# Kernel optimization log

Measured on AMD Instinct MI355X. Metric: run time of the kernel, lower is better.

## Reference

```python
import jax, jax.numpy as jnp
import numpy as np

N_USERS = 100000
N_ITEMS = 50000
N = N_USERS + N_ITEMS
EMBED_DIM = 64
N_LAYERS = 3
N_EDGES = 4800000


def setup_inputs() -> dict:
    key = jax.random.key(0)
    k1, k2, k3, k4, k5 = jax.random.split(key, 5)
    adj_row = jax.random.randint(k1, (N_EDGES,), 0, N, dtype=jnp.int64 if jax.config.jax_enable_x64 else jnp.int32)
    adj_col = jax.random.randint(k2, (N_EDGES,), 0, N, dtype=jnp.int64 if jax.config.jax_enable_x64 else jnp.int32)
    adj_val = jax.random.uniform(k3, (N_EDGES,), dtype=jnp.float32)
    # learned parameters: nn.init.normal_(std=0.1)
    user_emb = 0.1 * jax.random.normal(k4, (N_USERS, EMBED_DIM), dtype=jnp.float32)
    item_emb = 0.1 * jax.random.normal(k5, (N_ITEMS, EMBED_DIM), dtype=jnp.float32)
    return {"adj_row": adj_row, "adj_col": adj_col, "adj_val": adj_val,
            "user_emb": user_emb, "item_emb": item_emb}


def _spmm(row, col, val, x):
    # sparse (COO) matmul: out[r] += val * x[c]
    return jax.ops.segment_sum(val[:, None] * x[col], row, num_segments=N)


def reference(adj_row, adj_col, adj_val, user_emb, item_emb):
    emb = jnp.concatenate([user_emb, item_emb], axis=0)  # [N, D]
    acc = emb
    cur = emb
    for _ in range(N_LAYERS):
        cur = _spmm(adj_row, adj_col, adj_val, cur)
        acc = acc + cur
    out = acc / (N_LAYERS + 1)  # mean over stacked layer embeddings
    return out[:N_USERS], out[N_USERS:]
```

## Files before the change

kernel.cpp:

```cpp
#include <hip/hip_runtime.h>

#define N_USERS 100000
#define N_ITEMS 50000
#define N_NODES 150000
#define EMBED_DIM 64
#define N_EDGES 4800000
#define N_LAYERS 3

#define CB_SHIFT 9
#define CB_ROWS (1 << CB_SHIFT)
#define NC ((N_NODES + CB_ROWS - 1) >> CB_SHIFT)

#define EPB 8192
#define NPB ((N_EDGES + EPB - 1) / EPB)
#define INIT_BLOCKS ((N_NODES * EMBED_DIM / 4 + 255) / 256)

__device__ __forceinline__ unsigned short f2bf(float f) {
    unsigned u = __float_as_uint(f);
    u += 0x7fffu + ((u >> 16) & 1u);
    return (unsigned short)(u >> 16);
}
__device__ __forceinline__ float bf2f(unsigned short h) {
    return __uint_as_float((unsigned)h << 16);
}

__global__ __launch_bounds__(256)
void k_hist_init(const int* __restrict__ row, int* __restrict__ blk_hist,
                 const float* __restrict__ user_emb,
                 const float* __restrict__ item_emb,
                 unsigned short* __restrict__ curb) {
    __shared__ int h[NC];
    int blk = blockIdx.x;
    if (blk < NPB) {
        for (int i = threadIdx.x; i < NC; i += 256) h[i] = 0;
        __syncthreads();
        int e0 = blk * EPB;
        int e1 = e0 + EPB; if (e1 > N_EDGES) e1 = N_EDGES;
        for (int e = e0 + threadIdx.x; e < e1; e += 256)
            atomicAdd(&h[row[e] >> CB_SHIFT], 1);
        __syncthreads();
        for (int i = threadIdx.x; i < NC; i += 256)
            blk_hist[blk * NC + i] = h[i];
    } else {
        int i = (blk - NPB) * 256 + threadIdx.x;
        const int total = N_NODES * EMBED_DIM / 4;
        if (i >= total) return;
        const int user_elems = N_USERS * EMBED_DIM / 4;
        float4 v;
        if (i < user_elems) v = ((const float4*)user_emb)[i];
        else                v = ((const float4*)item_emb)[i - user_elems];
        ushort4 o;
        o.x = f2bf(v.x); o.y = f2bf(v.y); o.z = f2bf(v.z); o.w = f2bf(v.w);
        ((ushort4*)curb)[i] = o;
    }
}

__global__ __launch_bounds__(512)
void k_scan2d(const int* __restrict__ bh,
              int* __restrict__ cbase,
              int* __restrict__ boff) {
    __shared__ int part[512];
    int t = threadIdx.x;
    int total = 0;
    if (t < NC)
        for (int blk = 0; blk < NPB; ++blk) total += bh[blk * NC + t];
    part[t] = total;
    __syncthreads();
    for (int o = 1; o < 512; o <<= 1) {
        int v = (t >= o) ? part[t - o] : 0;
        __syncthreads();
        part[t] += v;
        __syncthreads();
    }
    int base = t ? part[t - 1] : 0;
    if (t < NC) {
        cbase[t] = base;
        int run = base;
        for (int blk = 0; blk < NPB; ++blk) {
            boff[blk * NC + t] = run;
            run += bh[blk * NC + t];
        }
    }
    if (t == 0) cbase[NC] = N_EDGES;
}

__global__ __launch_bounds__(256)
void k_part_f(const int* __restrict__ row,
              const int* __restrict__ col,
              const int* __restrict__ valI,
              const int* __restrict__ boff,
              int2* __restrict__ edges) {
    __shared__ int off[NC];
    int blk = blockIdx.x;
    int e0 = blk * EPB;
    int e1 = e0 + EPB; if (e1 > N_EDGES) e1 = N_EDGES;
    for (int i = threadIdx.x; i < NC; i += 256)
        off[i] = boff[blk * NC + i];
    __syncthreads();
    for (int e = e0 + threadIdx.x; e < e1; e += 256) {
        int r = row[e];
        int cb = r >> CB_SHIFT;
        int p = atomicAdd(&off[cb], 1);
        edges[p] = make_int2((col[e] << CB_SHIFT) | (r & (CB_ROWS - 1)), valI[e]);
    }
}

__global__ __launch_bounds__(512)
void k_sort_c(const int* __restrict__ cbase,
              const int2* __restrict__ edges,
              int2* __restrict__ csr,
              int* __restrict__ rowptr) {
    __shared__ int h[CB_ROWS];
    __shared__ int off[CB_ROWS];
    int b = blockIdx.x;
    int seg0 = cbase[b], seg1 = cbase[b + 1];
    h[threadIdx.x] = 0;
    __syncthreads();
    for (int e = seg0 + threadIdx.x; e < seg1; e += 512)
        atomicAdd(&h[edges[e].x & (CB_ROWS - 1)], 1);
    __syncthreads();
    for (int o = 1; o < CB_ROWS; o <<= 1) {
        int t = (threadIdx.x >= o) ? h[threadIdx.x - o] : 0;
        __syncthreads();
        h[threadIdx.x] += t;
        __syncthreads();
    }
    int row0 = b << CB_SHIFT;
    int nrows = N_NODES - row0; if (nrows > CB_ROWS) nrows = CB_ROWS;
    int excl = threadIdx.x ? h[threadIdx.x - 1] : 0;
    off[threadIdx.x] = excl;
    if (threadIdx.x < nrows) rowptr[row0 + threadIdx.x] = seg0 + excl;
    __syncthreads();
    for (int e = seg0 + threadIdx.x; e < seg1; e += 512) {
        int2 ee = edges[e];
        int rl = ee.x & (CB_ROWS - 1);
        int p = atomicAdd(&off[rl], 1);
        csr[seg0 + p] = make_int2(ee.x >> CB_SHIFT, ee.y);
    }
    if (b == NC - 1 && threadIdx.x == 0) rowptr[N_NODES] = N_EDGES;
}

__device__ __forceinline__ float spmv_row(const int2* __restrict__ cv,
                                          const unsigned short* __restrict__ x,
                                          int start, int end, int lane) {
    float a0 = 0.f, a1 = 0.f, a2 = 0.f, a3 = 0.f;
    float a4 = 0.f, a5 = 0.f, a6 = 0.f, a7 = 0.f;
    int j = start;
    for (; j + 8 <= end; j += 8) {
        int2 e0 = cv[j + 0], e1 = cv[j + 1], e2 = cv[j + 2], e3 = cv[j + 3];
        int2 e4 = cv[j + 4], e5 = cv[j + 5], e6 = cv[j + 6], e7 = cv[j + 7];
        float x0 = bf2f(x[((size_t)e0.x << 6) + lane]);
        float x1 = bf2f(x[((size_t)e1.x << 6) + lane]);
        float x2 = bf2f(x[((size_t)e2.x << 6) + lane]);
        float x3 = bf2f(x[((size_t)e3.x << 6) + lane]);
        float x4 = bf2f(x[((size_t)e4.x << 6) + lane]);
        float x5 = bf2f(x[((size_t)e5.x << 6) + lane]);
        float x6 = bf2f(x[((size_t)e6.x << 6) + lane]);
        float x7 = bf2f(x[((size_t)e7.x << 6) + lane]);
        a0 += __int_as_float(e0.y) * x0;
        a1 += __int_as_float(e1.y) * x1;
        a2 += __int_as_float(e2.y) * x2;
        a3 += __int_as_float(e3.y) * x3;
        a4 += __int_as_float(e4.y) * x4;
        a5 += __int_as_float(e5.y) * x5;
        a6 += __int_as_float(e6.y) * x6;
        a7 += __int_as_float(e7.y) * x7;
    }
    if (j + 4 <= end) {
        int2 e0 = cv[j + 0], e1 = cv[j + 1], e2 = cv[j + 2], e3 = cv[j + 3];
        a0 += __int_as_float(e0.y) * bf2f(x[((size_t)e0.x << 6) + lane]);
        a1 += __int_as_float(e1.y) * bf2f(x[((size_t)e1.x << 6) + lane]);
        a2 += __int_as_float(e2.y) * bf2f(x[((size_t)e2.x << 6) + lane]);
        a3 += __int_as_float(e3.y) * bf2f(x[((size_t)e3.x << 6) + lane]);
        j += 4;
    }
    for (; j < end; ++j) {
        int2 e = cv[j];
        a0 += __int_as_float(e.y) * bf2f(x[((size_t)e.x << 6) + lane]);
    }
    return ((a0 + a1) + (a2 + a3)) + ((a4 + a5) + (a6 + a7));
}

__global__ __launch_bounds__(256)
void lgcn_spmv_mid(const int* __restrict__ rowptr,
                   const int2* __restrict__ cv,
                   const unsigned short* __restrict__ x,
                   unsigned short* __restrict__ nxt) {
    int t = blockIdx.x * blockDim.x + threadIdx.x;
    int wave = t >> 6;
    int lane = t & 63;
    if (wave >= N_NODES) return;
    int r = __builtin_amdgcn_readfirstlane(wave);
    float sum = spmv_row(cv, x, rowptr[r], rowptr[r + 1], lane);
    nxt[((size_t)r << 6) + lane] = f2bf(sum);
}

__global__ __launch_bounds__(256)
void lgcn_spmv_last(const int* __restrict__ rowptr,
                    const int2* __restrict__ cv,
                    const unsigned short* __restrict__ x,
                    const unsigned short* __restrict__ e1,
                    const float* __restrict__ user_emb,
                    const float* __restrict__ item_emb,
                    float* __restrict__ out) {
    int t = blockIdx.x * blockDim.x + threadIdx.x;
    int wave = t >> 6;
    int lane = t & 63;
    if (wave >= N_NODES) return;
    int r = __builtin_amdgcn_readfirstlane(wave);
    float sum = spmv_row(cv, x, rowptr[r], rowptr[r + 1], lane);
    size_t o = ((size_t)r << 6) + lane;
    float e0 = (r < N_USERS) ? user_emb[o]
                             : item_emb[o - ((size_t)N_USERS << 6)];
    float v = ((e0 + bf2f(e1[o])) + bf2f(x[o])) + sum;
    out[o] = v * 0.25f;
}

__global__ void lgcn_init(const float* __restrict__ user_emb,
                          const float* __restrict__ item_emb,
                          float* __restrict__ cur,
                          float* __restrict__ acc) {
    int i = blockIdx.x * blockDim.x + threadIdx.x;
    const int total = N_NODES * EMBED_DIM / 4;
    if (i >= total) return;
    const int user_elems = N_USERS * EMBED_DIM / 4;
    float4 v;
    if (i < user_elems) v = ((const float4*)user_emb)[i];
    else                v = ((const float4*)item_emb)[i - user_elems];
    ((float4*)cur)[i] = v;
    ((float4*)acc)[i] = v;
}

__global__ void lgcn_spmm_atomic(const int* __restrict__ row,
                                 const int* __restrict__ col,
                                 const float* __restrict__ val,
                                 const float* __restrict__ x,
                                 float* __restrict__ y) {
    long long t = (long long)blockIdx.x * blockDim.x + threadIdx.x;
    int e = (int)(t >> 6);
    int d = (int)(t & 63);
    if (e >= N_EDGES) return;
    atomicAdd(&y[(long long)row[e] * EMBED_DIM + d],
              val[e] * x[(long long)col[e] * EMBED_DIM + d]);
}

__global__ void lgcn_accum(const float* __restrict__ cur,
                           float* __restrict__ acc, float s) {
    int i = blockIdx.x * blockDim.x + threadIdx.x;
    const int total = N_NODES * EMBED_DIM / 4;
    if (i >= total) return;
    float4 a = ((const float4*)acc)[i];
    float4 c = ((const float4*)cur)[i];
    a.x = (a.x + c.x) * s; a.y = (a.y + c.y) * s;
    a.z = (a.z + c.z) * s; a.w = (a.w + c.w) * s;
    ((float4*)acc)[i] = a;
}

extern "C" void kernel_launch(void* const* d_in, const int* in_sizes, int n_in,
                              void* d_out, int out_size, void* d_ws, size_t ws_size,
                              hipStream_t stream) {
    const int*   adj_row  = (const int*)d_in[0];
    const int*   adj_col  = (const int*)d_in[1];
    const float* adj_val  = (const float*)d_in[2];
    const int*   adj_valI = (const int*)d_in[2];
    const float* user_emb = (const float*)d_in[3];
    const float* item_emb = (const float*)d_in[4];
    float* out = (float*)d_out;

    const size_t buf_elems = (size_t)N_NODES * EMBED_DIM;

    char* wp = (char*)d_ws;
    int* cbase  = (int*)wp;  wp += (size_t)(NC + 1) * sizeof(int);
    int* rowptr = (int*)wp;  wp += (size_t)(N_NODES + 1) * sizeof(int);
    wp = (char*)(((size_t)wp + 63) & ~(size_t)63);
    int2* edges  = (int2*)wp; wp += (size_t)N_EDGES * sizeof(int2);
    wp = (char*)(((size_t)wp + 63) & ~(size_t)63);
    int2* csr_cv = (int2*)wp; wp += (size_t)N_EDGES * sizeof(int2);
    wp = (char*)(((size_t)wp + 63) & ~(size_t)63);
    unsigned short* curb = (unsigned short*)wp; wp += buf_elems * sizeof(unsigned short);
    unsigned short* nxtb = (unsigned short*)wp; wp += buf_elems * sizeof(unsigned short);
    size_t needed = (size_t)(wp - (char*)d_ws);
    int* blk_hist = (int*)csr_cv;
    int* boff     = blk_hist + (size_t)NPB * NC;
    unsigned short* e2b = (unsigned short*)edges;

    if (needed <= ws_size) {
        k_hist_init<<<NPB + INIT_BLOCKS, 256, 0, stream>>>(adj_row, blk_hist,
                                                           user_emb, item_emb, curb);
        k_scan2d<<<1, 512, 0, stream>>>(blk_hist, cbase, boff);
        k_part_f<<<NPB, 256, 0, stream>>>(adj_row, adj_col, adj_valI, boff, edges);
        k_sort_c<<<NC, 512, 0, stream>>>(cbase, edges, csr_cv, rowptr);

        const long long tthreads = (long long)N_NODES * 64;
        const int nblk = (int)((tthreads + 255) / 256);
        lgcn_spmv_mid<<<nblk, 256, 0, stream>>>(rowptr, csr_cv, curb, nxtb);
        lgcn_spmv_mid<<<nblk, 256, 0, stream>>>(rowptr, csr_cv, nxtb, e2b);
        lgcn_spmv_last<<<nblk, 256, 0, stream>>>(rowptr, csr_cv, e2b, nxtb,
                                                 user_emb, item_emb, out);
    } else {
        float* curF = (float*)d_ws;
        float* nxtF = curF + buf_elems;
        const int total = N_NODES * EMBED_DIM / 4;
        lgcn_init<<<(total + 255) / 256, 256, 0, stream>>>(user_emb, item_emb, curF, out);
        float* a = curF; float* b = nxtF;
        for (int layer = 0; layer < N_LAYERS; ++layer) {
            hipMemsetAsync(b, 0, buf_elems * sizeof(float), stream);
            long long tthr = (long long)N_EDGES * 64;
            lgcn_spmm_atomic<<<(unsigned)((tthr + 255) / 256), 256, 0, stream>>>(
                adj_row, adj_col, adj_val, a, b);
            float s = (layer == N_LAYERS - 1) ? (1.0f / (N_LAYERS + 1)) : 1.0f;
            lgcn_accum<<<(total + 255) / 256, 256, 0, stream>>>(b, out, s);
            float* t = a; a = b; b = t;
        }
    }
}
```

Baseline: 490.7 us.

## Pack CSR column and 14-bit edge value into one 32-bit word

Each CSR entry shrinks from an int2 (column plus fp32 value) to a single 32-bit word holding an 18-bit column index and a 14-bit compressed float (4-bit exponent, 10-bit mantissa, tiny values flushed to zero). This halves the edge-stream traffic read by each of the three SpMV passes, and the inner loop is unrolled to 16 edges per step. In exchange, edge weights lose precision, values below the exponent range become zero, and the decode adds ALU work per edge.

```diff
diff --git a/kernel.cpp b/kernel.cpp
--- a/kernel.cpp
+++ b/kernel.cpp
@@ -22,6 +22,18 @@
 }
 __device__ __forceinline__ float bf2f(unsigned short h) {
     return __uint_as_float((unsigned)h << 16);
+}
+
+__device__ __forceinline__ unsigned enc_val14(unsigned vbits) {
+    unsigned r = vbits + 0x1000u;
+    unsigned exp = (r >> 23) & 0xffu;
+    if (exp < 112u) return 0u;
+    return ((exp - 112u) << 10) | ((r >> 13) & 0x3ffu);
+}
+__device__ __forceinline__ float dec_val14(unsigned p) {
+    unsigned p14 = p & 0x3fffu;
+    unsigned bits = (((p14 >> 10) + 112u) << 23) | ((p14 & 0x3ffu) << 13);
+    return (p14 == 0u) ? 0.0f : __uint_as_float(bits);
 }
 
 __global__ __launch_bounds__(256)
@@ -108,7 +120,7 @@
 __global__ __launch_bounds__(512)
 void k_sort_c(const int* __restrict__ cbase,
               const int2* __restrict__ edges,
-              int2* __restrict__ csr,
+              unsigned* __restrict__ csr,
               int* __restrict__ rowptr) {
     __shared__ int h[CB_ROWS];
     __shared__ int off[CB_ROWS];
@@ -135,55 +147,79 @@
         int2 ee = edges[e];
         int rl = ee.x & (CB_ROWS - 1);
         int p = atomicAdd(&off[rl], 1);
-        csr[seg0 + p] = make_int2(ee.x >> CB_SHIFT, ee.y);
+        unsigned colv = (unsigned)(ee.x >> CB_SHIFT);
+        csr[seg0 + p] = (colv << 14) | enc_val14((unsigned)ee.y);
     }
     if (b == NC - 1 && threadIdx.x == 0) rowptr[N_NODES] = N_EDGES;
 }
 
-__device__ __forceinline__ float spmv_row(const int2* __restrict__ cv,
+__device__ __forceinline__ float spmv_row(const unsigned* __restrict__ cv,
                                           const unsigned short* __restrict__ x,
                                           int start, int end, int lane) {
     float a0 = 0.f, a1 = 0.f, a2 = 0.f, a3 = 0.f;
     float a4 = 0.f, a5 = 0.f, a6 = 0.f, a7 = 0.f;
     int j = start;
-    for (; j + 8 <= end; j += 8) {
-        int2 e0 = cv[j + 0], e1 = cv[j + 1], e2 = cv[j + 2], e3 = cv[j + 3];
-        int2 e4 = cv[j + 4], e5 = cv[j + 5], e6 = cv[j + 6], e7 = cv[j + 7];
-        float x0 = bf2f(x[((size_t)e0.x << 6) + lane]);
-        float x1 = bf2f(x[((size_t)e1.x << 6) + lane]);
-        float x2 = bf2f(x[((size_t)e2.x << 6) + lane]);
-        float x3 = bf2f(x[((size_t)e3.x << 6) + lane]);
-        float x4 = bf2f(x[((size_t)e4.x << 6) + lane]);
-        float x5 = bf2f(x[((size_t)e5.x << 6) + lane]);
-        float x6 = bf2f(x[((size_t)e6.x << 6) + lane]);
-        float x7 = bf2f(x[((size_t)e7.x << 6) + lane]);
-        a0 += __int_as_float(e0.y) * x0;
-        a1 += __int_as_float(e1.y) * x1;
-        a2 += __int_as_float(e2.y) * x2;
-        a3 += __int_as_float(e3.y) * x3;
-        a4 += __int_as_float(e4.y) * x4;
-        a5 += __int_as_float(e5.y) * x5;
-        a6 += __int_as_float(e6.y) * x6;
-        a7 += __int_as_float(e7.y) * x7;
+    for (; j + 16 <= end; j += 16) {
+        unsigned p0 = cv[j + 0],  p1 = cv[j + 1],  p2 = cv[j + 2],  p3 = cv[j + 3];
+        unsigned p4 = cv[j + 4],  p5 = cv[j + 5],  p6 = cv[j + 6],  p7 = cv[j + 7];
+        unsigned p8 = cv[j + 8],  p9 = cv[j + 9],  pa = cv[j + 10], pb = cv[j + 11];
+        unsigned pc = cv[j + 12], pd = cv[j + 13], pe = cv[j + 14], pf = cv[j + 15];
+        float x0 = bf2f(x[((size_t)(p0 >> 14) << 6) + lane]);
+        float x1 = bf2f(x[((size_t)(p1 >> 14) << 6) + lane]);
+        float x2 = bf2f(x[((size_t)(p2 >> 14) << 6) + lane]);
+        float x3 = bf2f(x[((size_t)(p3 >> 14) << 6) + lane]);
+        float x4 = bf2f(x[((size_t)(p4 >> 14) << 6) + lane]);
+        float x5 = bf2f(x[((size_t)(p5 >> 14) << 6) + lane]);
+        float x6 = bf2f(x[((size_t)(p6 >> 14) << 6) + lane]);
+        float x7 = bf2f(x[((size_t)(p7 >> 14) << 6) + lane]);
+        float x8 = bf2f(x[((size_t)(p8 >> 14) << 6) + lane]);
+        float x9 = bf2f(x[((size_t)(p9 >> 14) << 6) + lane]);
+        float xa = bf2f(x[((size_t)(pa >> 14) << 6) + lane]);
+        float xb = bf2f(x[((size_t)(pb >> 14) << 6) + lane]);
+        float xc = bf2f(x[((size_t)(pc >> 14) << 6) + lane]);
+        float xd = bf2f(x[((size_t)(pd >> 14) << 6) + lane]);
+        float xe = bf2f(x[((size_t)(pe >> 14) << 6) + lane]);
+        float xf = bf2f(x[((size_t)(pf >> 14) << 6) + lane]);
+        a0 += dec_val14(p0) * x0;  a1 += dec_val14(p1) * x1;
+        a2 += dec_val14(p2) * x2;  a3 += dec_val14(p3) * x3;
+        a4 += dec_val14(p4) * x4;  a5 += dec_val14(p5) * x5;
+        a6 += dec_val14(p6) * x6;  a7 += dec_val14(p7) * x7;
+        a0 += dec_val14(p8) * x8;  a1 += dec_val14(p9) * x9;
+        a2 += dec_val14(pa) * xa;  a3 += dec_val14(pb) * xb;
+        a4 += dec_val14(pc) * xc;  a5 += dec_val14(pd) * xd;
+        a6 += dec_val14(pe) * xe;  a7 += dec_val14(pf) * xf;
+    }
+    if (j + 8 <= end) {
+        unsigned p0 = cv[j + 0], p1 = cv[j + 1], p2 = cv[j + 2], p3 = cv[j + 3];
+        unsigned p4 = cv[j + 4], p5 = cv[j + 5], p6 = cv[j + 6], p7 = cv[j + 7];
+        a0 += dec_val14(p0) * bf2f(x[((size_t)(p0 >> 14) << 6) + lane]);
+        a1 += dec_val14(p1) * bf2f(x[((size_t)(p1 >> 14) << 6) + lane]);
+        a2 += dec_val14(p2) * bf2f(x[((size_t)(p2 >> 14) << 6) + lane]);
+        a3 += dec_val14(p3) * bf2f(x[((size_t)(p3 >> 14) << 6) + lane]);
+        a4 += dec_val14(p4) * bf2f(x[((size_t)(p4 >> 14) << 6) + lane]);
+        a5 += dec_val14(p5) * bf2f(x[((size_t)(p5 >> 14) << 6) + lane]);
+        a6 += dec_val14(p6) * bf2f(x[((size_t)(p6 >> 14) << 6) + lane]);
+        a7 += dec_val14(p7) * bf2f(x[((size_t)(p7 >> 14) << 6) + lane]);
+        j += 8;
     }
     if (j + 4 <= end) {
-        int2 e0 = cv[j + 0], e1 = cv[j + 1], e2 = cv[j + 2], e3 = cv[j + 3];
-        a0 += __int_as_float(e0.y) * bf2f(x[((size_t)e0.x << 6) + lane]);
-        a1 += __int_as_float(e1.y) * bf2f(x[((size_t)e1.x << 6) + lane]);
-        a2 += __int_as_float(e2.y) * bf2f(x[((size_t)e2.x << 6) + lane]);
-        a3 += __int_as_float(e3.y) * bf2f(x[((size_t)e3.x << 6) + lane]);
+        unsigned p0 = cv[j + 0], p1 = cv[j + 1], p2 = cv[j + 2], p3 = cv[j + 3];
+        a0 += dec_val14(p0) * bf2f(x[((size_t)(p0 >> 14) << 6) + lane]);
+        a1 += dec_val14(p1) * bf2f(x[((size_t)(p1 >> 14) << 6) + lane]);
+        a2 += dec_val14(p2) * bf2f(x[((size_t)(p2 >> 14) << 6) + lane]);
+        a3 += dec_val14(p3) * bf2f(x[((size_t)(p3 >> 14) << 6) + lane]);
         j += 4;
     }
     for (; j < end; ++j) {
-        int2 e = cv[j];
-        a0 += __int_as_float(e.y) * bf2f(x[((size_t)e.x << 6) + lane]);
+        unsigned p = cv[j];
+        a0 += dec_val14(p) * bf2f(x[((size_t)(p >> 14) << 6) + lane]);
     }
     return ((a0 + a1) + (a2 + a3)) + ((a4 + a5) + (a6 + a7));
 }
 
 __global__ __launch_bounds__(256)
 void lgcn_spmv_mid(const int* __restrict__ rowptr,
-                   const int2* __restrict__ cv,
+                   const unsigned* __restrict__ cv,
                    const unsigned short* __restrict__ x,
                    unsigned short* __restrict__ nxt) {
     int t = blockIdx.x * blockDim.x + threadIdx.x;
@@ -197,7 +233,7 @@
 
 __global__ __launch_bounds__(256)
 void lgcn_spmv_last(const int* __restrict__ rowptr,
-                    const int2* __restrict__ cv,
+                    const unsigned* __restrict__ cv,
                     const unsigned short* __restrict__ x,
                     const unsigned short* __restrict__ e1,
                     const float* __restrict__ user_emb,
@@ -275,12 +311,12 @@
     wp = (char*)(((size_t)wp + 63) & ~(size_t)63);
     int2* edges  = (int2*)wp; wp += (size_t)N_EDGES * sizeof(int2);
     wp = (char*)(((size_t)wp + 63) & ~(size_t)63);
-    int2* csr_cv = (int2*)wp; wp += (size_t)N_EDGES * sizeof(int2);
+    unsigned* csr = (unsigned*)wp; wp += (size_t)N_EDGES * sizeof(unsigned);
     wp = (char*)(((size_t)wp + 63) & ~(size_t)63);
     unsigned short* curb = (unsigned short*)wp; wp += buf_elems * sizeof(unsigned short);
     unsigned short* nxtb = (unsigned short*)wp; wp += buf_elems * sizeof(unsigned short);
     size_t needed = (size_t)(wp - (char*)d_ws);
-    int* blk_hist = (int*)csr_cv;
+    int* blk_hist = (int*)csr;
     int* boff     = blk_hist + (size_t)NPB * NC;
     unsigned short* e2b = (unsigned short*)edges;
 
@@ -289,13 +325,13 @@
                                                            user_emb, item_emb, curb);
         k_scan2d<<<1, 512, 0, stream>>>(blk_hist, cbase, boff);
         k_part_f<<<NPB, 256, 0, stream>>>(adj_row, adj_col, adj_valI, boff, edges);
-        k_sort_c<<<NC, 512, 0, stream>>>(cbase, edges, csr_cv, rowptr);
+        k_sort_c<<<NC, 512, 0, stream>>>(cbase, edges, csr, rowptr);
 
         const long long tthreads = (long long)N_NODES * 64;
         const int nblk = (int)((tthreads + 255) / 256);
-        lgcn_spmv_mid<<<nblk, 256, 0, stream>>>(rowptr, csr_cv, curb, nxtb);
-        lgcn_spmv_mid<<<nblk, 256, 0, stream>>>(rowptr, csr_cv, nxtb, e2b);
-        lgcn_spmv_last<<<nblk, 256, 0, stream>>>(rowptr, csr_cv, e2b, nxtb,
+        lgcn_spmv_mid<<<nblk, 256, 0, stream>>>(rowptr, csr, curb, nxtb);
+        lgcn_spmv_mid<<<nblk, 256, 0, stream>>>(rowptr, csr, nxtb, e2b);
+        lgcn_spmv_last<<<nblk, 256, 0, stream>>>(rowptr, csr, e2b, nxtb,
                                                  user_emb, item_emb, out);
     } else {
         float* curF = (float*)d_ws;
```

Result: faster. 453.0 us (-7.7%).
